# Kernel tuning notes

Measured on AMD Instinct MI355X. Metric: run time of the kernel, lower is better.

Reference implementation:

```python
import jax, jax.numpy as jnp
import numpy as np

N, E, G = 50000, 800000, 64
IN, EDGE = 128, 16
HID, H = 32, 4
FHID, HF = 64, 4
OUT = 16
NEG_SLOPE = 0.2


def _segment_softmax(logits, seg, num):
    m = jax.ops.segment_max(logits, seg, num_segments=num)
    m = jnp.where(jnp.isfinite(m), m, 0.0)
    p = jnp.exp(logits - m[seg])
    s = jax.ops.segment_sum(p, seg, num_segments=num)
    return p / (s[seg] + 1e-16)


def gatv2(x, src, dst, eattr, Wl, bl, Wr, br, We, att, bias, concat):
    # PyG GATv2Conv with add_self_loops=True (edge_attr fill_value='mean')
    n = x.shape[0]
    heads, ch = att.shape
    ones = jnp.ones((src.shape[0],), x.dtype)
    cnt = jax.ops.segment_sum(ones, dst, num_segments=n)
    mean_attr = jax.ops.segment_sum(eattr, dst, num_segments=n) / jnp.maximum(cnt, 1.0)[:, None]
    loop = jnp.arange(n)
    s = jnp.concatenate([src, loop])
    d = jnp.concatenate([dst, loop])
    ea = jnp.concatenate([eattr, mean_attr], axis=0)
    xl = (x @ Wl + bl).reshape(n, heads, ch)   # lin_l (source)
    xr = (x @ Wr + br).reshape(n, heads, ch)   # lin_r (target)
    ee = (ea @ We).reshape(-1, heads, ch)      # lin_edge (no bias)
    z = jax.nn.leaky_relu(xl[s] + xr[d] + ee, NEG_SLOPE)  # [E+N, H, C]
    logits = jnp.einsum('ehc,hc->eh', z, att)
    alpha = _segment_softmax(logits, d, n)
    out = jax.ops.segment_sum(alpha[:, :, None] * xl[s], d, num_segments=n)  # [N, H, C]
    out = out.reshape(n, heads * ch) if concat else out.mean(axis=1)
    return out + bias


def _forward(x, edge_attr, src, dst, batch,
             Wl0, bl0, Wr0, br0, We0, att0, bo0,
             Wlh, blh, Wrh, brh, Weh, atth, boh,
             Wlf, blf, Wrf, brf, Wef, attf, bof,
             Wlin, blin):
    h1 = jax.nn.relu(gatv2(x, src, dst, edge_attr, Wl0, bl0, Wr0, br0, We0, att0, bo0, True))
    h2 = jax.nn.relu(gatv2(h1, src, dst, edge_attr, Wlh, blh, Wrh, brh, Weh, atth, boh, True))
    h3 = jax.nn.relu(gatv2(h2, src, dst, edge_attr, Wlf, blf, Wrf, brf, Wef, attf, bof, False))
    # global_mean_pool over graphs
    gsum = jax.ops.segment_sum(h3, batch, num_segments=G)
    gcnt = jax.ops.segment_sum(jnp.ones((h3.shape[0],), h3.dtype), batch, num_segments=G)
    g = gsum / jnp.maximum(gcnt, 1.0)[:, None]
    return g @ Wlin + blin  # final_dropout inactive in eval mode


def setup_inputs():
    key = jax.random.key(0)
    ks = jax.random.split(key, 20)
    def p(i, shape, fan_in):
        return jax.random.normal(ks[i], shape, jnp.float32) / np.sqrt(fan_in)
    z = lambda *s: jnp.zeros(s, jnp.float32)
    return {
        'x': jax.random.normal(ks[0], (N, IN), jnp.float32),
        'edge_index': jax.random.randint(ks[1], (2, E), 0, N),
        'batch': jnp.sort(jax.random.randint(ks[2], (N,), 0, G)),
        'edge_attr': jax.random.normal(ks[3], (E, EDGE), jnp.float32),
        'Wl0': p(4, (IN, H * HID), IN), 'bl0': z(H * HID),
        'Wr0': p(5, (IN, H * HID), IN), 'br0': z(H * HID),
        'We0': p(6, (EDGE, H * HID), EDGE), 'att0': p(7, (H, HID), HID), 'bo0': z(H * HID),
        'Wlh': p(8, (H * HID, H * HID), H * HID), 'blh': z(H * HID),
        'Wrh': p(9, (H * HID, H * HID), H * HID), 'brh': z(H * HID),
        'Weh': p(10, (EDGE, H * HID), EDGE), 'atth': p(11, (H, HID), HID), 'boh': z(H * HID),
        'Wlf': p(12, (H * HID, HF * FHID), H * HID), 'blf': z(HF * FHID),
        'Wrf': p(13, (H * HID, HF * FHID), H * HID), 'brf': z(HF * FHID),
        'Wef': p(14, (EDGE, HF * FHID), EDGE), 'attf': p(15, (HF, FHID), FHID), 'bof': z(FHID),
        'Wlin': p(16, (FHID, OUT), FHID), 'blin': z(OUT),
    }


def reference(x, edge_index, batch, edge_attr, Wl0, bl0, Wr0, br0, We0, att0, bo0, Wlh, blh, Wrh, brh, Weh, atth, boh, Wlf, blf, Wrf, brf, Wef, attf, bof, Wlin, blin):
    return _forward(x, edge_attr, edge_index[0], edge_index[1], batch,
                    Wl0, bl0, Wr0, br0, We0, att0, bo0,
                    Wlh, blh, Wrh, brh, Weh, atth, boh,
                    Wlf, blf, Wrf, brf, Wef, attf, bof,
                    Wlin, blin)
```

## Files before the change

### kernel.cpp

```cpp
#include <hip/hip_runtime.h>
#include <cstddef>

#define NSLOPE 0.2f

constexpr int NN = 50000;
constexpr int EE = 800000;
constexpr int GG = 64;
constexpr int SCAN_B = 1024;

typedef unsigned short ushort_t;
typedef unsigned int uint_t;
typedef __bf16 bhalf;
typedef bhalf bhalf8 __attribute__((ext_vector_type(8)));
typedef float floatx4 __attribute__((ext_vector_type(4)));
typedef _Float16 half_t;
typedef half_t half2_t __attribute__((ext_vector_type(2)));

__device__ __forceinline__ ushort_t f2b(float f) {
  unsigned int u = __float_as_uint(f);
  unsigned int r = (u + 0x7fffu + ((u >> 16) & 1u)) >> 16;
  return (ushort_t)r;
}
__device__ __forceinline__ float b2f(ushort_t b) {
  return __uint_as_float(((unsigned int)b) << 16);
}
__device__ __forceinline__ uint_t packh2(float a, float b) {
  half2_t h = {(half_t)a, (half_t)b};
  return __builtin_bit_cast(uint_t, h);
}
__device__ __forceinline__ float dot2acc(uint_t ea, half2_t w, float c) {
  half2_t a = __builtin_bit_cast(half2_t, ea);
#if __has_builtin(__builtin_amdgcn_fdot2)
  return __builtin_amdgcn_fdot2(a, w, c, false);
#else
  return c + (float)a.x * (float)w.x + (float)a.y * (float)w.y;
#endif
}
__device__ __forceinline__ float fexp2(float x) {
#if __has_builtin(__builtin_amdgcn_exp2f)
  return __builtin_amdgcn_exp2f(x);
#else
  return exp2f(x);
#endif
}

__device__ __forceinline__ float red16(float x) {
  int v = __builtin_bit_cast(int, x);
  x += __builtin_bit_cast(float, __builtin_amdgcn_update_dpp(0, v, 0xB1, 0xF, 0xF, true));
  v = __builtin_bit_cast(int, x);
  x += __builtin_bit_cast(float, __builtin_amdgcn_update_dpp(0, v, 0x4E, 0xF, 0xF, true));
  v = __builtin_bit_cast(int, x);
  x += __builtin_bit_cast(float, __builtin_amdgcn_update_dpp(0, v, 0x124, 0xF, 0xF, true));
  v = __builtin_bit_cast(int, x);
  x += __builtin_bit_cast(float, __builtin_amdgcn_update_dpp(0, v, 0x128, 0xF, 0xF, true));
  return x;
}

__global__ void hist_kernel(const int* __restrict__ dst, int* __restrict__ hist, int E) {
  int e = blockIdx.x * blockDim.x + threadIdx.x;
  if (e < E) atomicAdd(&hist[dst[e]], 1);
}

__global__ void scan_block_kernel(const int* __restrict__ in, int* __restrict__ out,
                                  int* __restrict__ bsum, int n) {
  __shared__ int tmp[SCAN_B];
  int gid = blockIdx.x * SCAN_B + threadIdx.x;
  int v = (gid < n) ? in[gid] : 0;
  tmp[threadIdx.x] = v;
  __syncthreads();
  for (int off = 1; off < SCAN_B; off <<= 1) {
    int t = (threadIdx.x >= off) ? tmp[threadIdx.x - off] : 0;
    __syncthreads();
    tmp[threadIdx.x] += t;
    __syncthreads();
  }
  if (gid < n) out[gid] = tmp[threadIdx.x];
  if (threadIdx.x == SCAN_B - 1) bsum[blockIdx.x] = tmp[threadIdx.x];
}

__global__ void scan_totals_kernel(const int* __restrict__ bsum, int* __restrict__ boff, int nb) {
  if (blockIdx.x == 0 && threadIdx.x == 0) {
    int run = 0;
    for (int i = 0; i < nb; ++i) { boff[i] = run; run += bsum[i]; }
  }
}

__global__ void add_offsets_kernel(int* __restrict__ rowptr, const int* __restrict__ boff,
                                   int* __restrict__ cursor, int n) {
  int gid = blockIdx.x * SCAN_B + threadIdx.x;
  if (gid == 0) { rowptr[0] = 0; cursor[0] = 0; }
  if (gid < n) {
    int v = rowptr[1 + gid] + boff[blockIdx.x];
    rowptr[1 + gid] = v;
    if (1 + gid < n) cursor[1 + gid] = v;
  }
}

__global__ void scatter_fused_kernel(const int* __restrict__ dst, const int* __restrict__ src,
                                     const float* __restrict__ eattr, int* __restrict__ cursor,
                                     int* __restrict__ srcp, uint_t* __restrict__ eah, int E) {
  int e = blockIdx.x * blockDim.x + threadIdx.x;
  if (e >= E) return;
  const float4* a = reinterpret_cast<const float4*>(eattr + (size_t)e * 16);
  float4 f0 = a[0], f1 = a[1], f2 = a[2], f3 = a[3];
  int pos = atomicAdd(&cursor[dst[e]], 1);
  srcp[pos] = src[e];
  uint4 o0 = make_uint4(packh2(f0.x, f0.y), packh2(f0.z, f0.w),
                        packh2(f1.x, f1.y), packh2(f1.z, f1.w));
  uint4 o1 = make_uint4(packh2(f2.x, f2.y), packh2(f2.z, f2.w),
                        packh2(f3.x, f3.y), packh2(f3.z, f3.w));
  uint4* b = reinterpret_cast<uint4*>(eah + (size_t)pos * 8);
  b[0] = o0; b[1] = o1;
}

__global__ __launch_bounds__(256) void mean_attr_kernel(
    const int* __restrict__ rowptr, const uint_t* __restrict__ eah,
    uint_t* __restrict__ meanattr_h, int N) {
  const int lane = threadIdx.x & 63;
  int d = blockIdx.x * (blockDim.x >> 6) + (threadIdx.x >> 6);
  if (d >= N) return;
  int beg = rowptr[d], end = rowptr[d + 1];
  int k2 = lane & 7;
  int sub = lane >> 3;
  float ax = 0.f, ay = 0.f;
  for (int j = beg + sub; j < end; j += 8) {
    half2_t h = __builtin_bit_cast(half2_t, eah[(size_t)j * 8 + k2]);
    ax += (float)h.x; ay += (float)h.y;
  }
  ax += __shfl_xor(ax, 8);  ay += __shfl_xor(ay, 8);
  ax += __shfl_xor(ax, 16); ay += __shfl_xor(ay, 16);
  ax += __shfl_xor(ax, 32); ay += __shfl_xor(ay, 32);
  if (sub == 0) {
    int c = end - beg; if (c < 1) c = 1;
    float inv = 1.f / (float)c;
    meanattr_h[(size_t)d * 8 + k2] = packh2(ax * inv, ay * inv);
  }
}

__global__ void prep_w_kernel(const float* W0, ushort_t* T0, int n0,
                              const float* W1, ushort_t* T1, int n1,
                              const float* W2, ushort_t* T2, int n2,
                              const float* W3, ushort_t* T3, int n3,
                              const float* W4, ushort_t* T4, int n4,
                              const float* W5, ushort_t* T5, int n5) {
  const float* W; ushort_t* T; int Nc;
  switch (blockIdx.y) {
    case 0: W = W0; T = T0; Nc = n0; break;
    case 1: W = W1; T = T1; Nc = n1; break;
    case 2: W = W2; T = T2; Nc = n2; break;
    case 3: W = W3; T = T3; Nc = n3; break;
    case 4: W = W4; T = T4; Nc = n4; break;
    default: W = W5; T = T5; Nc = n5; break;
  }
  int idx = blockIdx.x * blockDim.x + threadIdx.x;
  if (idx >= Nc * 128) return;
  int n = idx >> 7, k = idx & 127;
  T[idx] = f2b(W[(size_t)k * Nc + n]);
}

__global__ void prep_we_kernel(const float* We0, const float* att0, uint_t* w0, float* a0,
                               const float* We1, const float* att1, uint_t* w1, float* a1,
                               const float* We2, const float* att2, uint_t* w2, float* a2) {
  const float* We; const float* att; uint_t* wp; float* ap; int C;
  switch (blockIdx.y) {
    case 0: We = We0; att = att0; wp = w0; ap = a0; C = 128; break;
    case 1: We = We1; att = att1; wp = w1; ap = a1; C = 128; break;
    default: We = We2; att = att2; wp = w2; ap = a2; C = 256; break;
  }
  int idx = blockIdx.x * blockDim.x + threadIdx.x;
  if (idx >= 9 * C) return;
  if (idx < 8 * C) {
    int sh = (C == 256) ? 8 : 7;
    int k2 = idx >> sh, ch = idx & (C - 1);
    wp[idx] = packh2(We[(size_t)(2 * k2) * C + ch], We[(size_t)(2 * k2 + 1) * C + ch]);
  } else {
    int ch = idx - 8 * C;
    ap[ch] = att[ch] * 1.44269504f;
  }
}

template <typename TA>
__global__ __launch_bounds__(256) void gemm_bt_dual_bf16(
    const TA* __restrict__ Xb,
    const ushort_t* __restrict__ Wt0, const float* __restrict__ b0, ushort_t* __restrict__ Y0,
    const ushort_t* __restrict__ Wt1, const float* __restrict__ b1, ushort_t* __restrict__ Y1,
    int M, int Nc) {
  constexpr int K = 128, BM = 128, LDT = 136;
  __shared__ ushort_t Als[BM * LDT];
  __shared__ ushort_t Bls[BM * LDT];
  int nb = Nc >> 7;
  int half = blockIdx.y / nb;
  int cb = blockIdx.y % nb;
  const ushort_t* Wt = half ? Wt1 : Wt0;
  const float* bias = half ? b1 : b0;
  ushort_t* Y = half ? Y1 : Y0;
  int r0 = blockIdx.x * BM;
  int col0 = cb * 128;
  int tid = threadIdx.x;
  {
    int rl = tid >> 5;
    int kq = (tid & 31) * 4;
#pragma unroll
    for (int s = 0; s < 16; ++s) {
      int row = rl + s * 8;
      int grow = r0 + row;
      ushort4 v = make_ushort4(0, 0, 0, 0);
      if (grow < M) {
        if constexpr (sizeof(TA) == 4) {
          float4 f = *reinterpret_cast<const float4*>(Xb + (size_t)grow * K + kq);
          v = make_ushort4(f2b(f.x), f2b(f.y), f2b(f.z), f2b(f.w));
        } else {
          v = *reinterpret_cast<const ushort4*>(Xb + (size_t)grow * K + kq);
        }
      }
      *reinterpret_cast<ushort4*>(&Als[row * LDT + kq]) = v;
      ushort4 wv = *reinterpret_cast<const ushort4*>(Wt + (size_t)(col0 + row) * K + kq);
      *reinterpret_cast<ushort4*>(&Bls[row * LDT + kq]) = wv;
    }
  }
  __syncthreads();
  int lane = tid & 63;
  int w = tid >> 6;
  int m0 = (w >> 1) * 64;
  int n0 = (w & 1) * 64;
  int rin = lane & 15, quad = lane >> 4;
  floatx4 acc[4][4];
#pragma unroll
  for (int i = 0; i < 4; ++i)
#pragma unroll
    for (int j = 0; j < 4; ++j) acc[i][j] = (floatx4){0.f, 0.f, 0.f, 0.f};
#pragma unroll
  for (int kt = 0; kt < 4; ++kt) {
    int ko = kt * 32 + quad * 8;
    bhalf8 af[4], bf[4];
#pragma unroll
    for (int i = 0; i < 4; ++i)
      af[i] = *reinterpret_cast<const bhalf8*>(&Als[(m0 + i * 16 + rin) * LDT + ko]);
#pragma unroll
    for (int i = 0; i < 4; ++i)
      bf[i] = *reinterpret_cast<const bhalf8*>(&Bls[(n0 + i * 16 + rin) * LDT + ko]);
#pragma unroll
    for (int mi = 0; mi < 4; ++mi)
#pragma unroll
      for (int ni = 0; ni < 4; ++ni)
        acc[mi][ni] = __builtin_amdgcn_mfma_f32_16x16x32_bf16(af[mi], bf[ni], acc[mi][ni], 0, 0, 0);
  }
#pragma unroll
  for (int ni = 0; ni < 4; ++ni) {
    int gcol = col0 + n0 + ni * 16 + rin;
    float bb = bias[gcol];
#pragma unroll
    for (int mi = 0; mi < 4; ++mi) {
      int growb = r0 + m0 + mi * 16 + quad * 4;
#pragma unroll
      for (int r = 0; r < 4; ++r) {
        int grow = growb + r;
        if (grow < M) Y[(size_t)grow * Nc + gcol] = f2b(acc[mi][ni][r] + bb);
      }
    }
  }
}

template <int VPL>
__device__ __forceinline__ void loadb(const ushort_t* p, float* v) {
  if constexpr (VPL == 2) {
    ushort2 t = *reinterpret_cast<const ushort2*>(p);
    v[0] = b2f(t.x); v[1] = b2f(t.y);
  } else {
    ushort4 t = *reinterpret_cast<const ushort4*>(p);
    v[0] = b2f(t.x); v[1] = b2f(t.y); v[2] = b2f(t.z); v[3] = b2f(t.w);
  }
}
template <int VPL>
__device__ __forceinline__ void storeb(ushort_t* p, const float* v) {
  if constexpr (VPL == 2) {
    *reinterpret_cast<ushort2*>(p) = make_ushort2(f2b(v[0]), f2b(v[1]));
  } else {
    *reinterpret_cast<ushort4*>(p) = make_ushort4(f2b(v[0]), f2b(v[1]), f2b(v[2]), f2b(v[3]));
  }
}

template <int VPL>
__device__ __forceinline__ float lrelu_dot(const float* xv, const float* rv,
                                           const half2_t (*wepk)[VPL], const float* areg,
                                           const uint_t* ea) {
  float part = 0.f;
#pragma unroll
  for (int j = 0; j < VPL; ++j) {
    float z = xv[j] + rv[j];
#pragma unroll
    for (int k2 = 0; k2 < 8; ++k2) z = dot2acc(ea[k2], wepk[k2][j], z);
    float zl = fmaxf(z, NSLOPE * z);
    part = fmaf(zl, areg[j], part);
  }
  return red16(part);
}

template <int EB, int VPL, int C>
__device__ __forceinline__ void process_group(
    const int* __restrict__ srcp, const uint_t* __restrict__ eah, int j,
    const ushort_t* __restrict__ xl, int lane, const float* rv,
    const half2_t (*wepk)[VPL], const float* areg,
    float& s, float* acc) {
  int sn[EB];
#pragma unroll
  for (int u = 0; u < EB; ++u) sn[u] = srcp[j + u];
  float xv[EB][VPL];
#pragma unroll
  for (int u = 0; u < EB; ++u) loadb<VPL>(xl + (size_t)sn[u] * C + lane * VPL, xv[u]);
  float lg[EB];
#pragma unroll
  for (int u = 0; u < EB; ++u) {
    const uint4* ap4 = reinterpret_cast<const uint4*>(eah + (size_t)(j + u) * 8);
    uint4 e0 = ap4[0], e1 = ap4[1];
    uint_t ea[8] = {e0.x, e0.y, e0.z, e0.w, e1.x, e1.y, e1.z, e1.w};
    lg[u] = lrelu_dot<VPL>(xv[u], rv, wepk, areg, ea);
  }
  float p[EB], ps = 0.f;
#pragma unroll
  for (int u = 0; u < EB; ++u) { p[u] = fexp2(lg[u]); ps += p[u]; }
  s += ps;
#pragma unroll
  for (int jj = 0; jj < VPL; ++jj) {
    float t = p[0] * xv[0][jj];
#pragma unroll
    for (int u = 1; u < EB; ++u) t = fmaf(p[u], xv[u][jj], t);
    acc[jj] += t;
  }
}

template <int VPL, int C>
__device__ __forceinline__ void process_edge(
    int sn, const uint_t* ea,
    const ushort_t* __restrict__ xl, int lane, const float* rv,
    const half2_t (*wepk)[VPL], const float* areg,
    float& s, float* acc) {
  float xv[VPL];
  loadb<VPL>(xl + (size_t)sn * C + lane * VPL, xv);
  float lg = lrelu_dot<VPL>(xv, rv, wepk, areg, ea);
  float p = fexp2(lg);
  s += p;
#pragma unroll
  for (int jj = 0; jj < VPL; ++jj) acc[jj] = fmaf(p, xv[jj], acc[jj]);
}

template <int C, bool FINAL>
__global__ __launch_bounds__(64) void gat_fused_kernel(
    const int* __restrict__ rowptr,
    const int* __restrict__ srcp, const uint_t* __restrict__ eah,
    const uint_t* __restrict__ meanattr_h,
    const ushort_t* __restrict__ xl, const ushort_t* __restrict__ xr,
    const uint_t* __restrict__ wep,
    const float* __restrict__ atts,
    const float* __restrict__ bias, ushort_t* __restrict__ hout, int N) {
  constexpr int VPL = C / 64;
  const int lane = threadIdx.x & 63;
  int d = blockIdx.x;
  if (d >= N) return;

  half2_t wepk[8][VPL];
  float areg[VPL];
#pragma unroll
  for (int k2 = 0; k2 < 8; ++k2)
#pragma unroll
    for (int jj = 0; jj < VPL; ++jj)
      wepk[k2][jj] = __builtin_bit_cast(half2_t, wep[k2 * C + lane * VPL + jj]);
#pragma unroll
  for (int jj = 0; jj < VPL; ++jj) areg[jj] = atts[lane * VPL + jj];

  int beg = rowptr[d], end = rowptr[d + 1];
  float rv[VPL];
  loadb<VPL>(xr + (size_t)d * C + lane * VPL, rv);

  float s = 0.f;
  float acc[VPL];
#pragma unroll
  for (int jj = 0; jj < VPL; ++jj) acc[jj] = 0.f;

  int j = beg;
  if constexpr (C == 128) {
    for (; j + 8 <= end; j += 8)
      process_group<8, VPL, C>(srcp, eah, j, xl, lane, rv, wepk, areg, s, acc);
  }
  for (; j + 4 <= end; j += 4)
    process_group<4, VPL, C>(srcp, eah, j, xl, lane, rv, wepk, areg, s, acc);
  for (; j + 2 <= end; j += 2)
    process_group<2, VPL, C>(srcp, eah, j, xl, lane, rv, wepk, areg, s, acc);
  for (; j < end; ++j)
    process_group<1, VPL, C>(srcp, eah, j, xl, lane, rv, wepk, areg, s, acc);

  {
    const uint4* mp4 = reinterpret_cast<const uint4*>(meanattr_h + (size_t)d * 8);
    uint4 e0 = mp4[0], e1 = mp4[1];
    uint_t ea[8] = {e0.x, e0.y, e0.z, e0.w, e1.x, e1.y, e1.z, e1.w};
    process_edge<VPL, C>(d, ea, xl, lane, rv, wepk, areg, s, acc);
  }

  float inv = 1.f / (s + 1e-16f);
  if constexpr (!FINAL) {
    float res[VPL];
#pragma unroll
    for (int jj = 0; jj < VPL; ++jj) {
      float v = acc[jj] * inv + bias[lane * VPL + jj];
      res[jj] = v > 0.f ? v : 0.f;
    }
    storeb<VPL>(hout + (size_t)d * C + lane * VPL, res);
  } else {
    float v[VPL];
#pragma unroll
    for (int jj = 0; jj < VPL; ++jj) v[jj] = acc[jj] * inv;
#pragma unroll
    for (int jj = 0; jj < VPL; ++jj) {
      v[jj] += __shfl_xor(v[jj], 16);
      v[jj] += __shfl_xor(v[jj], 32);
    }
    if (lane < 16) {
      float res[VPL];
#pragma unroll
      for (int jj = 0; jj < VPL; ++jj) {
        float val = 0.25f * v[jj] + bias[lane * VPL + jj];
        res[jj] = val > 0.f ? val : 0.f;
      }
      storeb<VPL>(hout + (size_t)d * 64 + lane * VPL, res);
    }
  }
}

__global__ __launch_bounds__(256) void pool_kernel(
    const ushort_t* __restrict__ h3, const int* __restrict__ batch,
    float* __restrict__ gsum, float* __restrict__ gcnt, int N) {
  const int lane = threadIdx.x & 63;
  const int w = blockIdx.x * (blockDim.x >> 6) + (threadIdx.x >> 6);
  const int nw = gridDim.x * (blockDim.x >> 6);
  const int chunk = (N + nw - 1) / nw;
  int i0 = w * chunk;
  int i1 = i0 + chunk; if (i1 > N) i1 = N;
  if (i0 >= i1) return;
  int cur = batch[i0];
  float acc = 0.f;
  int cnt = 0;
  for (int i = i0; i < i1; ++i) {
    int g = batch[i];
    if (g != cur) {
      atomicAdd(&gsum[(size_t)cur * 64 + lane], acc);
      if (lane == 0) atomicAdd(&gcnt[cur], (float)cnt);
      acc = 0.f; cnt = 0; cur = g;
    }
    acc += b2f(h3[(size_t)i * 64 + lane]);
    ++cnt;
  }
  atomicAdd(&gsum[(size_t)cur * 64 + lane], acc);
  if (lane == 0) atomicAdd(&gcnt[cur], (float)cnt);
}

__global__ void final_kernel(const float* __restrict__ gsum, const float* __restrict__ gcnt,
                             const float* __restrict__ Wlin, const float* __restrict__ blin,
                             float* __restrict__ out) {
  int idx = blockIdx.x * blockDim.x + threadIdx.x;
  if (idx >= GG * 16) return;
  int g = idx >> 4, o = idx & 15;
  float c = gcnt[g];
  c = c > 1.f ? c : 1.f;
  float inv = 1.f / c;
  float acc = blin[o];
  for (int f = 0; f < 64; ++f) acc = fmaf(gsum[(size_t)g * 64 + f] * inv, Wlin[f * 16 + o], acc);
  out[idx] = acc;
}

extern "C" void kernel_launch(void* const* d_in, const int* in_sizes, int n_in,
                              void* d_out, int out_size, void* d_ws, size_t ws_size,
                              hipStream_t stream) {
  (void)in_sizes; (void)n_in; (void)out_size; (void)ws_size;
  const float* x     = (const float*)d_in[0];
  const int*   eidx  = (const int*)d_in[1];
  const int*   batch = (const int*)d_in[2];
  const float* eattr = (const float*)d_in[3];
  const float* Wl0 = (const float*)d_in[4];  const float* bl0 = (const float*)d_in[5];
  const float* Wr0 = (const float*)d_in[6];  const float* br0 = (const float*)d_in[7];
  const float* We0 = (const float*)d_in[8];  const float* att0 = (const float*)d_in[9];
  const float* bo0 = (const float*)d_in[10];
  const float* Wlh = (const float*)d_in[11]; const float* blh = (const float*)d_in[12];
  const float* Wrh = (const float*)d_in[13]; const float* brh = (const float*)d_in[14];
  const float* Weh = (const float*)d_in[15]; const float* atth = (const float*)d_in[16];
  const float* boh = (const float*)d_in[17];
  const float* Wlf = (const float*)d_in[18]; const float* blf = (const float*)d_in[19];
  const float* Wrf = (const float*)d_in[20]; const float* brf = (const float*)d_in[21];
  const float* Wef = (const float*)d_in[22]; const float* attf = (const float*)d_in[23];
  const float* bof = (const float*)d_in[24];
  const float* Wlin = (const float*)d_in[25]; const float* blin = (const float*)d_in[26];

  const int* src = eidx;
  const int* dst = eidx + EE;

  char* ws = (char*)d_ws;
  size_t off = 0;
  auto take = [&](size_t bytes) -> void* {
    void* p = ws + off;
    off += (bytes + 1023) & ~(size_t)1023;
    return p;
  };
  ushort_t* xl     = (ushort_t*)take((size_t)NN * 256 * 2);
  ushort_t* xr     = (ushort_t*)take((size_t)NN * 256 * 2);
  ushort_t* hb     = (ushort_t*)take((size_t)NN * 128 * 2);
  uint_t* meanattr_h = (uint_t*)take((size_t)NN * 8 * 4);
  int* hist        = (int*)take((size_t)NN * 4);
  float* gsum      = (float*)take((size_t)GG * 64 * 4);
  float* gcnt      = (float*)take((size_t)GG * 4);
  int* rowptr      = (int*)take((size_t)(NN + 1) * 4);
  int* cursor      = (int*)take((size_t)NN * 4);
  int* bsum        = (int*)take(256);
  int* boff        = (int*)take(256);
  ushort_t* wtl0   = (ushort_t*)take((size_t)128 * 128 * 2);
  ushort_t* wtr0   = (ushort_t*)take((size_t)128 * 128 * 2);
  ushort_t* wtlh   = (ushort_t*)take((size_t)128 * 128 * 2);
  ushort_t* wtrh   = (ushort_t*)take((size_t)128 * 128 * 2);
  ushort_t* wtlf   = (ushort_t*)take((size_t)256 * 128 * 2);
  ushort_t* wtrf   = (ushort_t*)take((size_t)256 * 128 * 2);
  int* srcp        = (int*)take((size_t)EE * 4);
  uint_t* eah      = (uint_t*)take((size_t)EE * 8 * 4);
  uint_t* we0p     = (uint_t*)take((size_t)8 * 128 * 4);
  uint_t* wehp     = (uint_t*)take((size_t)8 * 128 * 4);
  uint_t* wefp     = (uint_t*)take((size_t)8 * 256 * 4);
  float* att0s     = (float*)take((size_t)128 * 4);
  float* atths     = (float*)take((size_t)128 * 4);
  float* attfs     = (float*)take((size_t)256 * 4);

  hipMemsetAsync(hist, 0, 200704 + 16384 + 256, stream);
  hist_kernel<<<(EE + 255) / 256, 256, 0, stream>>>(dst, hist, EE);
  int nsb = (NN + SCAN_B - 1) / SCAN_B;
  scan_block_kernel<<<nsb, SCAN_B, 0, stream>>>(hist, rowptr + 1, bsum, NN);
  scan_totals_kernel<<<1, 64, 0, stream>>>(bsum, boff, nsb);
  add_offsets_kernel<<<nsb, SCAN_B, 0, stream>>>(rowptr, boff, cursor, NN);
  scatter_fused_kernel<<<(EE + 255) / 256, 256, 0, stream>>>(dst, src, eattr, cursor, srcp, eah, EE);
  mean_attr_kernel<<<(NN + 3) / 4, 256, 0, stream>>>(rowptr, eah, meanattr_h, NN);
  prep_w_kernel<<<dim3(128, 6), 256, 0, stream>>>(Wl0, wtl0, 128, Wr0, wtr0, 128,
                                                  Wlh, wtlh, 128, Wrh, wtrh, 128,
                                                  Wlf, wtlf, 256, Wrf, wtrf, 256);
  prep_we_kernel<<<dim3(9, 3), 256, 0, stream>>>(We0, att0, we0p, att0s,
                                                 Weh, atth, wehp, atths,
                                                 Wef, attf, wefp, attfs);

  const int GEMM_MB = (NN + 127) / 128;

  gemm_bt_dual_bf16<float><<<dim3(GEMM_MB, 2), 256, 0, stream>>>(
      x, wtl0, bl0, xl, wtr0, br0, xr, NN, 128);
  gat_fused_kernel<128, false><<<NN, 64, 0, stream>>>(
      rowptr, srcp, eah, meanattr_h, xl, xr, we0p, att0s, bo0, hb, NN);
  gemm_bt_dual_bf16<ushort_t><<<dim3(GEMM_MB, 2), 256, 0, stream>>>(
      hb, wtlh, blh, xl, wtrh, brh, xr, NN, 128);
  gat_fused_kernel<128, false><<<NN, 64, 0, stream>>>(
      rowptr, srcp, eah, meanattr_h, xl, xr, wehp, atths, boh, hb, NN);
  gemm_bt_dual_bf16<ushort_t><<<dim3(GEMM_MB, 4), 256, 0, stream>>>(
      hb, wtlf, blf, xl, wtrf, brf, xr, NN, 256);
  gat_fused_kernel<256, true><<<NN, 64, 0, stream>>>(
      rowptr, srcp, eah, meanattr_h, xl, xr, wefp, attfs, bof, hb, NN);
  pool_kernel<<<128, 256, 0, stream>>>(hb, batch, gsum, gcnt, NN);
  final_kernel<<<4, 256, 0, stream>>>(gsum, gcnt, Wlin, blin, (float*)d_out);
}
```

Baseline: 663.9 us.

## Trim preprocessing launches, split edge scatter, reuse A tile across dual GEMM

Merges the scan-totals step into add_offsets using a wave reduction, and merges the two weight-prep kernels into one launch. The histogram now handles four edges per thread through an int4 load. The edge scatter is split into a position/permutation pass and a separate pass that builds the half-precision edge attributes. The dual GEMM loads the A tile once and loops over both weight matrices, halving the grid. These cut launch count and redundant A loads, at the cost of an extra perm buffer, an extra kernel pass and less GEMM parallelism.

```diff
diff --git a/kernel.cpp b/kernel.cpp
--- a/kernel.cpp
+++ b/kernel.cpp
@@ -56,9 +56,14 @@
   return x;
 }
 
-__global__ void hist_kernel(const int* __restrict__ dst, int* __restrict__ hist, int E) {
-  int e = blockIdx.x * blockDim.x + threadIdx.x;
-  if (e < E) atomicAdd(&hist[dst[e]], 1);
+__global__ void hist_kernel(const int* __restrict__ dst, int* __restrict__ hist, int E4) {
+  int i = blockIdx.x * blockDim.x + threadIdx.x;
+  if (i >= E4) return;
+  int4 d = reinterpret_cast<const int4*>(dst)[i];
+  atomicAdd(&hist[d.x], 1);
+  atomicAdd(&hist[d.y], 1);
+  atomicAdd(&hist[d.z], 1);
+  atomicAdd(&hist[d.w], 1);
 }
 
 __global__ void scan_block_kernel(const int* __restrict__ in, int* __restrict__ out,
@@ -78,33 +83,44 @@
   if (threadIdx.x == SCAN_B - 1) bsum[blockIdx.x] = tmp[threadIdx.x];
 }
 
-__global__ void scan_totals_kernel(const int* __restrict__ bsum, int* __restrict__ boff, int nb) {
-  if (blockIdx.x == 0 && threadIdx.x == 0) {
-    int run = 0;
-    for (int i = 0; i < nb; ++i) { boff[i] = run; run += bsum[i]; }
-  }
-}
-
-__global__ void add_offsets_kernel(int* __restrict__ rowptr, const int* __restrict__ boff,
-                                   int* __restrict__ cursor, int n) {
-  int gid = blockIdx.x * SCAN_B + threadIdx.x;
+__global__ void add_offsets_kernel(int* __restrict__ rowptr, const int* __restrict__ bsum,
+                                   int* __restrict__ cursor, int n, int nb) {
+  int lane = threadIdx.x & 63;
+  int bx = blockIdx.x;
+  int v = (lane < nb && lane < bx) ? bsum[lane] : 0;
+  v += __shfl_xor(v, 1);
+  v += __shfl_xor(v, 2);
+  v += __shfl_xor(v, 4);
+  v += __shfl_xor(v, 8);
+  v += __shfl_xor(v, 16);
+  v += __shfl_xor(v, 32);
+  int boff = v;
+  int gid = bx * SCAN_B + threadIdx.x;
   if (gid == 0) { rowptr[0] = 0; cursor[0] = 0; }
   if (gid < n) {
-    int v = rowptr[1 + gid] + boff[blockIdx.x];
-    rowptr[1 + gid] = v;
-    if (1 + gid < n) cursor[1 + gid] = v;
-  }
-}
-
-__global__ void scatter_fused_kernel(const int* __restrict__ dst, const int* __restrict__ src,
-                                     const float* __restrict__ eattr, int* __restrict__ cursor,
-                                     int* __restrict__ srcp, uint_t* __restrict__ eah, int E) {
+    int t = rowptr[1 + gid] + boff;
+    rowptr[1 + gid] = t;
+    if (1 + gid < n) cursor[1 + gid] = t;
+  }
+}
+
+__global__ void scatter_pos_kernel(const int* __restrict__ dst, const int* __restrict__ src,
+                                   int* __restrict__ cursor, int* __restrict__ srcp,
+                                   int* __restrict__ perm, int E) {
   int e = blockIdx.x * blockDim.x + threadIdx.x;
   if (e >= E) return;
+  int pos = atomicAdd(&cursor[dst[e]], 1);
+  srcp[pos] = src[e];
+  perm[pos] = e;
+}
+
+__global__ void eah_build_kernel(const int* __restrict__ perm, const float* __restrict__ eattr,
+                                 uint_t* __restrict__ eah, int E) {
+  int pos = blockIdx.x * blockDim.x + threadIdx.x;
+  if (pos >= E) return;
+  int e = perm[pos];
   const float4* a = reinterpret_cast<const float4*>(eattr + (size_t)e * 16);
   float4 f0 = a[0], f1 = a[1], f2 = a[2], f3 = a[3];
-  int pos = atomicAdd(&cursor[dst[e]], 1);
-  srcp[pos] = src[e];
   uint4 o0 = make_uint4(packh2(f0.x, f0.y), packh2(f0.z, f0.w),
                         packh2(f1.x, f1.y), packh2(f1.z, f1.w));
   uint4 o1 = make_uint4(packh2(f2.x, f2.y), packh2(f2.z, f2.w),
@@ -137,45 +153,46 @@
   }
 }
 
-__global__ void prep_w_kernel(const float* W0, ushort_t* T0, int n0,
-                              const float* W1, ushort_t* T1, int n1,
-                              const float* W2, ushort_t* T2, int n2,
-                              const float* W3, ushort_t* T3, int n3,
-                              const float* W4, ushort_t* T4, int n4,
-                              const float* W5, ushort_t* T5, int n5) {
-  const float* W; ushort_t* T; int Nc;
-  switch (blockIdx.y) {
-    case 0: W = W0; T = T0; Nc = n0; break;
-    case 1: W = W1; T = T1; Nc = n1; break;
-    case 2: W = W2; T = T2; Nc = n2; break;
-    case 3: W = W3; T = T3; Nc = n3; break;
-    case 4: W = W4; T = T4; Nc = n4; break;
-    default: W = W5; T = T5; Nc = n5; break;
-  }
+__global__ void prep_all_kernel(const float* W0, ushort_t* T0, int n0,
+                                const float* W1, ushort_t* T1, int n1,
+                                const float* W2, ushort_t* T2, int n2,
+                                const float* W3, ushort_t* T3, int n3,
+                                const float* W4, ushort_t* T4, int n4,
+                                const float* W5, ushort_t* T5, int n5,
+                                const float* We0, const float* att0, uint_t* w0, float* a0,
+                                const float* We1, const float* att1, uint_t* w1, float* a1,
+                                const float* We2, const float* att2, uint_t* w2, float* a2) {
   int idx = blockIdx.x * blockDim.x + threadIdx.x;
-  if (idx >= Nc * 128) return;
-  int n = idx >> 7, k = idx & 127;
-  T[idx] = f2b(W[(size_t)k * Nc + n]);
-}
-
-__global__ void prep_we_kernel(const float* We0, const float* att0, uint_t* w0, float* a0,
-                               const float* We1, const float* att1, uint_t* w1, float* a1,
-                               const float* We2, const float* att2, uint_t* w2, float* a2) {
-  const float* We; const float* att; uint_t* wp; float* ap; int C;
-  switch (blockIdx.y) {
-    case 0: We = We0; att = att0; wp = w0; ap = a0; C = 128; break;
-    case 1: We = We1; att = att1; wp = w1; ap = a1; C = 128; break;
-    default: We = We2; att = att2; wp = w2; ap = a2; C = 256; break;
-  }
-  int idx = blockIdx.x * blockDim.x + threadIdx.x;
-  if (idx >= 9 * C) return;
-  if (idx < 8 * C) {
-    int sh = (C == 256) ? 8 : 7;
-    int k2 = idx >> sh, ch = idx & (C - 1);
-    wp[idx] = packh2(We[(size_t)(2 * k2) * C + ch], We[(size_t)(2 * k2 + 1) * C + ch]);
+  int y = blockIdx.y;
+  if (y < 6) {
+    const float* W; ushort_t* T; int Nc;
+    switch (y) {
+      case 0: W = W0; T = T0; Nc = n0; break;
+      case 1: W = W1; T = T1; Nc = n1; break;
+      case 2: W = W2; T = T2; Nc = n2; break;
+      case 3: W = W3; T = T3; Nc = n3; break;
+      case 4: W = W4; T = T4; Nc = n4; break;
+      default: W = W5; T = T5; Nc = n5; break;
+    }
+    if (idx >= Nc * 128) return;
+    int n = idx >> 7, k = idx & 127;
+    T[idx] = f2b(W[(size_t)k * Nc + n]);
   } else {
-    int ch = idx - 8 * C;
-    ap[ch] = att[ch] * 1.44269504f;
+    const float* We; const float* att; uint_t* wp; float* ap; int C;
+    switch (y) {
+      case 6: We = We0; att = att0; wp = w0; ap = a0; C = 128; break;
+      case 7: We = We1; att = att1; wp = w1; ap = a1; C = 128; break;
+      default: We = We2; att = att2; wp = w2; ap = a2; C = 256; break;
+    }
+    if (idx >= 9 * C) return;
+    if (idx < 8 * C) {
+      int sh = (C == 256) ? 8 : 7;
+      int k2 = idx >> sh, ch = idx & (C - 1);
+      wp[idx] = packh2(We[(size_t)(2 * k2) * C + ch], We[(size_t)(2 * k2 + 1) * C + ch]);
+    } else {
+      int ch = idx - 8 * C;
+      ap[ch] = att[ch] * 1.44269504f;
+    }
   }
 }
 
@@ -188,74 +205,77 @@
   constexpr int K = 128, BM = 128, LDT = 136;
   __shared__ ushort_t Als[BM * LDT];
   __shared__ ushort_t Bls[BM * LDT];
-  int nb = Nc >> 7;
-  int half = blockIdx.y / nb;
-  int cb = blockIdx.y % nb;
-  const ushort_t* Wt = half ? Wt1 : Wt0;
-  const float* bias = half ? b1 : b0;
-  ushort_t* Y = half ? Y1 : Y0;
   int r0 = blockIdx.x * BM;
-  int col0 = cb * 128;
+  int col0 = blockIdx.y * 128;
   int tid = threadIdx.x;
-  {
-    int rl = tid >> 5;
-    int kq = (tid & 31) * 4;
-#pragma unroll
-    for (int s = 0; s < 16; ++s) {
-      int row = rl + s * 8;
-      int grow = r0 + row;
-      ushort4 v = make_ushort4(0, 0, 0, 0);
-      if (grow < M) {
-        if constexpr (sizeof(TA) == 4) {
-          float4 f = *reinterpret_cast<const float4*>(Xb + (size_t)grow * K + kq);
-          v = make_ushort4(f2b(f.x), f2b(f.y), f2b(f.z), f2b(f.w));
-        } else {
-          v = *reinterpret_cast<const ushort4*>(Xb + (size_t)grow * K + kq);
-        }
+  int rl = tid >> 5;
+  int kq = (tid & 31) * 4;
+#pragma unroll
+  for (int s = 0; s < 16; ++s) {
+    int row = rl + s * 8;
+    int grow = r0 + row;
+    ushort4 v = make_ushort4(0, 0, 0, 0);
+    if (grow < M) {
+      if constexpr (sizeof(TA) == 4) {
+        float4 f = *reinterpret_cast<const float4*>(Xb + (size_t)grow * K + kq);
+        v = make_ushort4(f2b(f.x), f2b(f.y), f2b(f.z), f2b(f.w));
+      } else {
+        v = *reinterpret_cast<const ushort4*>(Xb + (size_t)grow * K + kq);
       }
-      *reinterpret_cast<ushort4*>(&Als[row * LDT + kq]) = v;
-      ushort4 wv = *reinterpret_cast<const ushort4*>(Wt + (size_t)(col0 + row) * K + kq);
-      *reinterpret_cast<ushort4*>(&Bls[row * LDT + kq]) = wv;
-    }
-  }
-  __syncthreads();
+    }
+    *reinterpret_cast<ushort4*>(&Als[row * LDT + kq]) = v;
+  }
   int lane = tid & 63;
   int w = tid >> 6;
   int m0 = (w >> 1) * 64;
   int n0 = (w & 1) * 64;
   int rin = lane & 15, quad = lane >> 4;
-  floatx4 acc[4][4];
-#pragma unroll
-  for (int i = 0; i < 4; ++i)
-#pragma unroll
-    for (int j = 0; j < 4; ++j) acc[i][j] = (floatx4){0.f, 0.f, 0.f, 0.f};
-#pragma unroll
-  for (int kt = 0; kt < 4; ++kt) {
-    int ko = kt * 32 + quad * 8;
-    bhalf8 af[4], bf[4];
+
+  for (int half = 0; half < 2; ++half) {
+    const ushort_t* Wt = half ? Wt1 : Wt0;
+    const float* bias = half ? b1 : b0;
+    ushort_t* Y = half ? Y1 : Y0;
+    __syncthreads();
+#pragma unroll
+    for (int s = 0; s < 16; ++s) {
+      int row = rl + s * 8;
+      ushort4 wv = *reinterpret_cast<const ushort4*>(Wt + (size_t)(col0 + row) * K + kq);
+      *reinterpret_cast<ushort4*>(&Bls[row * LDT + kq]) = wv;
+    }
+    __syncthreads();
+    floatx4 acc[4][4];
 #pragma unroll
     for (int i = 0; i < 4; ++i)
-      af[i] = *reinterpret_cast<const bhalf8*>(&Als[(m0 + i * 16 + rin) * LDT + ko]);
-#pragma unroll
-    for (int i = 0; i < 4; ++i)
-      bf[i] = *reinterpret_cast<const bhalf8*>(&Bls[(n0 + i * 16 + rin) * LDT + ko]);
-#pragma unroll
-    for (int mi = 0; mi < 4; ++mi)
-#pragma unroll
-      for (int ni = 0; ni < 4; ++ni)
-        acc[mi][ni] = __builtin_amdgcn_mfma_f32_16x16x32_bf16(af[mi], bf[ni], acc[mi][ni], 0, 0, 0);
-  }
-#pragma unroll
-  for (int ni = 0; ni < 4; ++ni) {
-    int gcol = col0 + n0 + ni * 16 + rin;
-    float bb = bias[gcol];
-#pragma unroll
-    for (int mi = 0; mi < 4; ++mi) {
-      int growb = r0 + m0 + mi * 16 + quad * 4;
-#pragma unroll
-      for (int r = 0; r < 4; ++r) {
-        int grow = growb + r;
-        if (grow < M) Y[(size_t)grow * Nc + gcol] = f2b(acc[mi][ni][r] + bb);
+#pragma unroll
+      for (int j = 0; j < 4; ++j) acc[i][j] = (floatx4){0.f, 0.f, 0.f, 0.f};
+#pragma unroll
+    for (int kt = 0; kt < 4; ++kt) {
+      int ko = kt * 32 + quad * 8;
+      bhalf8 af[4], bf[4];
+#pragma unroll
+      for (int i = 0; i < 4; ++i)
+        af[i] = *reinterpret_cast<const bhalf8*>(&Als[(m0 + i * 16 + rin) * LDT + ko]);
+#pragma unroll
+      for (int i = 0; i < 4; ++i)
+        bf[i] = *reinterpret_cast<const bhalf8*>(&Bls[(n0 + i * 16 + rin) * LDT + ko]);
+#pragma unroll
+      for (int mi = 0; mi < 4; ++mi)
+#pragma unroll
+        for (int ni = 0; ni < 4; ++ni)
+          acc[mi][ni] = __builtin_amdgcn_mfma_f32_16x16x32_bf16(af[mi], bf[ni], acc[mi][ni], 0, 0, 0);
+    }
+#pragma unroll
+    for (int ni = 0; ni < 4; ++ni) {
+      int gcol = col0 + n0 + ni * 16 + rin;
+      float bb = bias[gcol];
+#pragma unroll
+      for (int mi = 0; mi < 4; ++mi) {
+        int growb = r0 + m0 + mi * 16 + quad * 4;
+#pragma unroll
+        for (int r = 0; r < 4; ++r) {
+          int grow = growb + r;
+          if (grow < M) Y[(size_t)grow * Nc + gcol] = f2b(acc[mi][ni][r] + bb);
+        }
       }
     }
   }
@@ -505,11 +525,10 @@
   uint_t* meanattr_h = (uint_t*)take((size_t)NN * 8 * 4);
   int* hist        = (int*)take((size_t)NN * 4);
   float* gsum      = (float*)take((size_t)GG * 64 * 4);
-  float* gcnt      = (float*)take((size_t)GG * 4);
+  float* gcnt     = (float*)take((size_t)GG * 4);
   int* rowptr      = (int*)take((size_t)(NN + 1) * 4);
   int* cursor      = (int*)take((size_t)NN * 4);
   int* bsum        = (int*)take(256);
-  int* boff        = (int*)take(256);
   ushort_t* wtl0   = (ushort_t*)take((size_t)128 * 128 * 2);
   ushort_t* wtr0   = (ushort_t*)take((size_t)128 * 128 * 2);
   ushort_t* wtlh   = (ushort_t*)take((size_t)128 * 128 * 2);
@@ -517,6 +536,7 @@
   ushort_t* wtlf   = (ushort_t*)take((size_t)256 * 128 * 2);
   ushort_t* wtrf   = (ushort_t*)take((size_t)256 * 128 * 2);
   int* srcp        = (int*)take((size_t)EE * 4);
+  int* perm        = (int*)take((size_t)EE * 4);
   uint_t* eah      = (uint_t*)take((size_t)EE * 8 * 4);
   uint_t* we0p     = (uint_t*)take((size_t)8 * 128 * 4);
   uint_t* wehp     = (uint_t*)take((size_t)8 * 128 * 4);
@@ -526,31 +546,29 @@
   float* attfs     = (float*)take((size_t)256 * 4);
 
   hipMemsetAsync(hist, 0, 200704 + 16384 + 256, stream);
-  hist_kernel<<<(EE + 255) / 256, 256, 0, stream>>>(dst, hist, EE);
+  hist_kernel<<<(EE / 4 + 255) / 256, 256, 0, stream>>>(dst, hist, EE / 4);
   int nsb = (NN + SCAN_B - 1) / SCAN_B;
   scan_block_kernel<<<nsb, SCAN_B, 0, stream>>>(hist, rowptr + 1, bsum, NN);
-  scan_totals_kernel<<<1, 64, 0, stream>>>(bsum, boff, nsb);
-  add_offsets_kernel<<<nsb, SCAN_B, 0, stream>>>(rowptr, boff, cursor, NN);
-  scatter_fused_kernel<<<(EE + 255) / 256, 256, 0, stream>>>(dst, src, eattr, cursor, srcp, eah, EE);
+  add_offsets_kernel<<<nsb, SCAN_B, 0, stream>>>(rowptr, bsum, cursor, NN, nsb);
+  scatter_pos_kernel<<<(EE + 255) / 256, 256, 0, stream>>>(dst, src, cursor, srcp, perm, EE);
+  eah_build_kernel<<<(EE + 255) / 256, 256, 0, stream>>>(perm, eattr, eah, EE);
   mean_attr_kernel<<<(NN + 3) / 4, 256, 0, stream>>>(rowptr, eah, meanattr_h, NN);
-  prep_w_kernel<<<dim3(128, 6), 256, 0, stream>>>(Wl0, wtl0, 128, Wr0, wtr0, 128,
-                                                  Wlh, wtlh, 128, Wrh, wtrh, 128,
-                                                  Wlf, wtlf, 256, Wrf, wtrf, 256);
-  prep_we_kernel<<<dim3(9, 3), 256, 0, stream>>>(We0, att0, we0p, att0s,
-                                                 Weh, atth, wehp, atths,
-                                                 Wef, attf, wefp, attfs);
+  prep_all_kernel<<<dim3(128, 9), 256, 0, stream>>>(
+      Wl0, wtl0, 128, Wr0, wtr0, 128, Wlh, wtlh, 128, Wrh, wtrh, 128,
+      Wlf, wtlf, 256, Wrf, wtrf, 256,
+      We0, att0, we0p, att0s, Weh, atth, wehp, atths, Wef, attf, wefp, attfs);
 
   const int GEMM_MB = (NN + 127) / 128;
 
-  gemm_bt_dual_bf16<float><<<dim3(GEMM_MB, 2), 256, 0, stream>>>(
+  gemm_bt_dual_bf16<float><<<dim3(GEMM_MB, 1), 256, 0, stream>>>(
       x, wtl0, bl0, xl, wtr0, br0, xr, NN, 128);
   gat_fused_kernel<128, false><<<NN, 64, 0, stream>>>(
       rowptr, srcp, eah, meanattr_h, xl, xr, we0p, att0s, bo0, hb, NN);
-  gemm_bt_dual_bf16<ushort_t><<<dim3(GEMM_MB, 2), 256, 0, stream>>>(
+  gemm_bt_dual_bf16<ushort_t><<<dim3(GEMM_MB, 1), 256, 0, stream>>>(
       hb, wtlh, blh, xl, wtrh, brh, xr, NN, 128);
   gat_fused_kernel<128, false><<<NN, 64, 0, stream>>>(
       rowptr, srcp, eah, meanattr_h, xl, xr, wehp, atths, boh, hb, NN);
-  gemm_bt_dual_bf16<ushort_t><<<dim3(GEMM_MB, 4), 256, 0, stream>>>(
+  gemm_bt_dual_bf16<ushort_t><<<dim3(GEMM_MB, 2), 256, 0, stream>>>(
       hb, wtlf, blf, xl, wtrf, brf, xr, NN, 256);
   gat_fused_kernel<256, true><<<NN, 64, 0, stream>>>(
       rowptr, srcp, eah, meanattr_h, xl, xr, wefp, attfs, bof, hb, NN);
```

After: 654.2 us. No clear change (-1.5%).
